# Kernel tuning notes

Measured on AMD Instinct MI355X. Metric: run time of the kernel, lower is better.

Reference implementation:

```python
import jax, jax.numpy as jnp
import numpy as np

D_INPUT, D_MODEL, D_OUTPUT, D_STATE, FACTOR = 100, 256, 100, 64, 2
N2 = D_STATE // 2  # complex conjugate-pair states (S4D)
B_SZ, L_SEQ = 16, 4096


def setup_inputs() -> dict:
    key = jax.random.key(0)
    ks = jax.random.split(key, 12)
    H, N = D_MODEL, N2
    # S4D ('diag-lin', zoh, real_transform='exp') parameters
    log_dt = jax.random.uniform(ks[0], (H,)) * (np.log(0.1) - np.log(0.001)) + np.log(0.001)
    log_A_real = jnp.log(0.5 * jnp.ones((H, N), jnp.float32))
    A_imag = jnp.pi * jnp.broadcast_to(jnp.arange(N, dtype=jnp.float32), (H, N))
    B_re = jnp.ones((H, N), jnp.float32)
    B_im = jnp.zeros((H, N), jnp.float32)
    C_re = jax.random.normal(ks[1], (H, N), jnp.float32)
    C_im = jax.random.normal(ks[2], (H, N), jnp.float32)
    Dskip = jax.random.normal(ks[3], (H,), jnp.float32)
    return {
        'x': jax.random.normal(ks[4], (B_SZ, L_SEQ, D_INPUT), jnp.float32),
        'enc_w': jax.random.normal(ks[5], (D_MODEL, D_INPUT), jnp.float32) / np.sqrt(D_INPUT),
        'enc_b': jnp.zeros((D_MODEL,), jnp.float32),
        'log_dt': log_dt, 'log_A_real': log_A_real, 'A_imag': A_imag,
        'B_re': B_re, 'B_im': B_im, 'C_re': C_re, 'C_im': C_im, 'Dskip': Dskip,
        'ln_g': jnp.ones((D_MODEL,), jnp.float32),
        'ln_b': jnp.zeros((D_MODEL,), jnp.float32),
        'dec1_w': jax.random.normal(ks[6], (D_MODEL * FACTOR, D_MODEL), jnp.float32) / np.sqrt(D_MODEL),
        'dec1_b': jnp.zeros((D_MODEL * FACTOR,), jnp.float32),
        'dec2_w': jax.random.normal(ks[7], (D_OUTPUT, D_MODEL * FACTOR), jnp.float32) / np.sqrt(D_MODEL * FACTOR),
        'dec2_b': jnp.zeros((D_OUTPUT,), jnp.float32),
    }


def s4d_kernel(log_dt, log_A_real, A_imag, B_re, B_im, C_re, C_im, L):
    # diagonal SSM kernel, ZOH discretization: K[h,l] = 2 Re sum_n C'_hn exp(dt_h A_hn)^l
    dt = jnp.exp(log_dt)[:, None]                      # (H,1)
    A = -jnp.exp(log_A_real) + 1j * A_imag             # (H,N)
    C = (B_re + 1j * B_im) * (C_re + 1j * C_im)        # (H,N), B folded into C
    dtA = dt * A                                       # (H,N)
    C = C * (jnp.exp(dtA) - 1.0) / A                   # ZOH correction
    V = jnp.exp(dtA[:, :, None] * jnp.arange(L))       # (H,N,L) Vandermonde
    return 2.0 * jnp.einsum('hn,hnl->hl', C, V).real   # (H,L)


def reference(x, enc_w, enc_b, log_dt, log_A_real, A_imag, B_re, B_im, C_re, C_im,
              Dskip, ln_g, ln_b, dec1_w, dec1_b, dec2_w, dec2_b):
    B, L, _ = x.shape
    u = (x @ enc_w.T + enc_b).transpose(0, 2, 1)       # (B,H,L)
    # FFTConv (single layer), dropout = identity (eval)
    k = s4d_kernel(log_dt, log_A_real, A_imag, B_re, B_im, C_re, C_im, L)
    n = 2 * L
    y = jnp.fft.irfft(jnp.fft.rfft(u, n=n) * jnp.fft.rfft(k, n=n)[None], n=n)[..., :L]
    y = y + u * Dskip[None, :, None]
    y = jax.nn.gelu(y, approximate=False)
    h = y + u                                          # residual
    # LayerNorm over channel dim
    t = h.transpose(0, 2, 1)                           # (B,L,H)
    mu = t.mean(-1, keepdims=True)
    var = jnp.mean((t - mu) ** 2, axis=-1, keepdims=True)
    t = (t - mu) / jnp.sqrt(var + 1e-5) * ln_g + ln_b
    # decoder MLP
    out = jax.nn.gelu(t @ dec1_w.T + dec1_b, approximate=False) @ dec2_w.T + dec2_b
    return out
```

## Files before the change

kernel.cpp:

```cpp
#include <hip/hip_runtime.h>
#include <hip/hip_bf16.h>

#define BB    16
#define LL    4096
#define DIN   100
#define HD    256
#define NN    32
#define DHID  512
#define DOUT  100
#define MROWS (BB*LL)
#define CH    64
#define CC    64
#define NCH   (BB*CC)

#define OFF_WRE    0
#define OFF_WIM    8192
#define OFF_KRE    16384
#define OFF_KIM    24576
#define OFF_WCHR   32768
#define OFF_WCHI   40960
#define OFF_ENCB   49152
#define OFF_DSK    49408
#define OFF_LNG    49664
#define OFF_LNB    49920
#define OFF_B1     50176
#define OFF_B2     50688
#define OFF_WENCB  50816
#define OFF_W1B    67200
#define OFF_W2B    132736
#define OFF_WFL    165504
#define OFF_BY     1230464
#define OFF_VST    2279040
#define OFF_UH     2803328
#define OFF_S      11191936
#define OFF_YH     19580544
#define OFF_TB     OFF_S
#define OFF_G0     OFF_UH
#define OFF_G1     OFF_YH
#define OFF_XB     OFF_YH

typedef __bf16 bf16x8 __attribute__((ext_vector_type(8)));
typedef float  f32x4  __attribute__((ext_vector_type(4)));

static __device__ __forceinline__ int probe_bf16(const void* lng) {
    return ((const unsigned int*)lng)[0] != 0x3f800000u;
}
static __device__ __forceinline__ float ldin(const void* p, long i, int isbf) {
    return isbf ? __bfloat162float(((const __hip_bfloat16*)p)[i]) : ((const float*)p)[i];
}
static __device__ __forceinline__ unsigned short f2bf(float v) {
    union { float f; unsigned u; } c; c.f = v;
    unsigned r = c.u + 0x7fffu + ((c.u >> 16) & 1u);
    return (unsigned short)(r >> 16);
}
static __device__ __forceinline__ float bf2f(unsigned short v) {
    union { unsigned u; float f; } c; c.u = ((unsigned)v) << 16; return c.f;
}
static __device__ __forceinline__ float gelu_f(float x) {
    float z  = fabsf(x) * 0.70710678118654752f;
    float tt = __builtin_amdgcn_rcpf(fmaf(0.3275911f, z, 1.0f));
    float p  = tt * fmaf(tt, fmaf(tt, fmaf(tt, fmaf(tt, 1.061405429f, -1.453152027f),
                          1.421413741f), -0.284496736f), 0.254829592f);
    float er = 1.0f - p * __expf(-z * z);
    return 0.5f * x * (1.0f + copysignf(er, x));
}
static __device__ __forceinline__ void gl2lds16(const unsigned short* g, unsigned short* l) {
    __builtin_amdgcn_global_load_lds(
        (const __attribute__((address_space(1))) unsigned int*)g,
        (__attribute__((address_space(3))) unsigned int*)l, 16, 0, 0);
}

__global__ __launch_bounds__(256) void k_prep(
    const void* encw, const void* encb, const void* logdt, const void* loga,
    const void* aim, const void* bre, const void* bim, const void* cre,
    const void* cim, const void* dsk, const void* lng, const void* lnb,
    const void* w1, const void* b1, const void* w2, const void* b2, float* ws)
{
    const int isbf = probe_bf16(lng);
    unsigned short* WEB = (unsigned short*)(ws + OFF_WENCB);
    unsigned short* W1B = (unsigned short*)(ws + OFF_W1B);
    unsigned short* W2B = (unsigned short*)(ws + OFF_W2B);
    const int total = 8192 + 256*4 + 512 + 128 + 32768 + 131072 + 65536;
    for (int idx = blockIdx.x * blockDim.x + threadIdx.x; idx < total;
         idx += gridDim.x * blockDim.x) {
        int i = idx;
        if (i < 8192) {
            int h = i >> 5;
            float dt  = expf(ldin(logdt, h, isbf));
            float Are = -expf(ldin(loga, i, isbf));
            float Aim = ldin(aim, i, isbf);
            float er  = expf(dt * Are);
            float sv, cv; sincosf(dt * Aim, &sv, &cv);
            float wre = er * cv, wim = er * sv;
            float Bre = ldin(bre, i, isbf), Bim = ldin(bim, i, isbf);
            float Cre = ldin(cre, i, isbf), Cim = ldin(cim, i, isbf);
            float C0re = Bre*Cre - Bim*Cim;
            float C0im = Bre*Cim + Bim*Cre;
            float inv = 1.0f / (Are*Are + Aim*Aim);
            float nre = wre - 1.0f, nim = wim;
            float Zre = (nre*Are + nim*Aim) * inv;
            float Zim = (nim*Are - nre*Aim) * inv;
            float kre = 2.0f * (C0re*Zre - C0im*Zim);
            float kim = -2.0f * (C0re*Zim + C0im*Zre);
            ws[OFF_WRE + i] = wre;  ws[OFF_WIM + i] = wim;
            ws[OFF_KRE + i] = kre;  ws[OFF_KIM + i] = kim;
            float* Wf = ws + OFF_WFL + (long)h * 4160 + 2*(i & 31);
            float pr = 1.0f, pi = 0.0f;
            for (int d = 0; d <= 64; ++d) {
                Wf[d*64]     = pr;
                Wf[d*64 + 1] = pi;
                float tr = pr*wre - pi*wim;
                pi = pr*wim + pi*wre; pr = tr;
            }
            ws[OFF_WCHR + i] = Wf[64*64];
            ws[OFF_WCHI + i] = Wf[64*64 + 1];
        } else if ((i -= 8192) < 256) {
            ws[OFF_ENCB + i] = ldin(encb, i, isbf);
        } else if ((i -= 256) < 256) {
            ws[OFF_DSK + i] = ldin(dsk, i, isbf);
        } else if ((i -= 256) < 256) {
            ws[OFF_LNG + i] = ldin(lng, i, isbf);
        } else if ((i -= 256) < 256) {
            ws[OFF_LNB + i] = ldin(lnb, i, isbf);
        } else if ((i -= 256) < 512) {
            ws[OFF_B1 + i] = ldin(b1, i, isbf);
        } else if ((i -= 512) < 128) {
            ws[OFF_B2 + i] = (i < 100) ? ldin(b2, i, isbf) : 0.0f;
        } else if ((i -= 128) < 32768) {
            int h = i >> 7, k = i & 127;
            WEB[i] = (k < 100) ? f2bf(ldin(encw, (long)h*100 + k, isbf)) : (unsigned short)0;
        } else if ((i -= 32768) < 131072) {
            W1B[i] = f2bf(ldin(w1, i, isbf));
        } else if ((i -= 131072) < 65536) {
            int j = i >> 9, k = i & 511;
            W2B[i] = (j < 100) ? f2bf(ldin(w2, (long)j*512 + k, isbf)) : (unsigned short)0;
        }
    }
}

__global__ __launch_bounds__(256) void k_xcvt(const void* x, const void* lng, float* ws)
{
    const int isbf = probe_bf16(lng);
    unsigned short* Xb = (unsigned short*)(ws + OFF_XB);
    const int total = 65536 * 16;
    for (int s = blockIdx.x * 256 + threadIdx.x; s < total; s += 1024 * 256) {
        int row = s >> 4, slot = s & 15;
        int k0 = slot * 8;
        unsigned short pk[8];
        if (!isbf) {
            const float* xr = (const float*)x + (long)row * 100;
            if (slot < 12) {
                float4 a = *(const float4*)(xr + k0);
                float4 b = *(const float4*)(xr + k0 + 4);
                pk[0]=f2bf(a.x); pk[1]=f2bf(a.y); pk[2]=f2bf(a.z); pk[3]=f2bf(a.w);
                pk[4]=f2bf(b.x); pk[5]=f2bf(b.y); pk[6]=f2bf(b.z); pk[7]=f2bf(b.w);
            } else if (slot == 12) {
                float4 a = *(const float4*)(xr + 96);
                pk[0]=f2bf(a.x); pk[1]=f2bf(a.y); pk[2]=f2bf(a.z); pk[3]=f2bf(a.w);
                pk[4]=0; pk[5]=0; pk[6]=0; pk[7]=0;
            } else {
                #pragma unroll
                for (int j = 0; j < 8; ++j) pk[j] = 0;
            }
        } else {
            const unsigned short* xr = (const unsigned short*)x + (long)row * 100;
            if (slot < 12) {
                *(uint2*)&pk[0] = *(const uint2*)(xr + k0);
                *(uint2*)&pk[4] = *(const uint2*)(xr + k0 + 4);
            } else if (slot == 12) {
                *(uint2*)&pk[0] = *(const uint2*)(xr + 96);
                pk[4]=0; pk[5]=0; pk[6]=0; pk[7]=0;
            } else {
                #pragma unroll
                for (int j = 0; j < 8; ++j) pk[j] = 0;
            }
        }
        *(float4*)&Xb[(long)row * 128 + k0] = *(const float4*)pk;
    }
}

__global__ __launch_bounds__(256) void k_tker(float* ws)
{
    __shared__ float Wp[65*65];
    __shared__ float kr[32], ki[32], Ks[64];
    int h = blockIdx.x;
    int t = threadIdx.x;
    for (int idx = t; idx < 4160; idx += 256) {
        int d = idx >> 6, c = idx & 63;
        Wp[d*65 + c] = ws[OFF_WFL + (long)h*4160 + idx];
    }
    if (t < 32) kr[t] = ws[OFF_KRE + h*32 + t];
    else if (t < 64) ki[t-32] = ws[OFF_KIM + h*32 + (t-32)];
    __syncthreads();
    if (t < 64) {
        float s = 0.0f;
        #pragma unroll
        for (int n = 0; n < 32; ++n)
            s += kr[n]*Wp[t*65 + 2*n] + ki[n]*Wp[t*65 + 2*n + 1];
        Ks[t] = s;
    }
    __syncthreads();
    unsigned short* BY = (unsigned short*)(ws + OFF_BY) + (long)h*8192;
    for (int idx = t; idx < 8192; idx += 256) {
        int j = idx >> 7, k = idx & 127;
        float v;
        if (k < 64) {
            v = (k <= j) ? Ks[j - k] : 0.0f;
        } else {
            int c = k - 64, n = c >> 1;
            float pr = Wp[(j+1)*65 + 2*n], pi = Wp[(j+1)*65 + 2*n + 1];
            v = ((c & 1) == 0) ? (kr[n]*pr + ki[n]*pi) : (ki[n]*pr - kr[n]*pi);
        }
        BY[idx] = f2bf(v);
    }
    unsigned short* Vst = (unsigned short*)(ws + OFF_VST) + (long)h*4096;
    for (int idx = t; idx < 4096; idx += 256) {
        int comp = idx >> 6, i = idx & 63;
        Vst[idx] = f2bf(Wp[(63 - i)*65 + comp]);
    }
}

__global__ __launch_bounds__(256) void k_encm(float* ws)
{
    __shared__ unsigned short SM[32768];
    unsigned short* Cs = SM;
    const unsigned short* Xb  = (const unsigned short*)(ws + OFF_XB);
    const unsigned short* WEB = (const unsigned short*)(ws + OFF_WENCB);
    int bid = blockIdx.x;
    int rt = bid >> 1, ct = bid & 1;
    long row0 = (long)rt * 128;
    int c0 = ct * 128;
    int t = threadIdx.x;
    int lane = t & 63, wv = t >> 6;
    int wm = (wv & 1) * 64, wn = (wv >> 1) * 64;
    int quad = lane >> 4, mr = lane & 15;
    int swz = lane & 7;
    int sr = t >> 3, sdst = (t & 7) * 8, ssrc = ((t & 7) ^ (sr & 7)) * 8;
    f32x4 acc[4][4] = {};
    #pragma unroll
    for (int it = 0; it < 4; ++it) {
        int r = sr + it * 32;
        gl2lds16(&Xb[(row0 + r) * 128 + ssrc], &SM[r * 64 + sdst]);
        gl2lds16(&WEB[(long)(c0 + r) * 128 + ssrc], &SM[8192 + r * 64 + sdst]);
    }
    __syncthreads();
    #pragma unroll
    for (int kc = 0; kc < 2; ++kc) {
        const unsigned short* As = &SM[(kc & 1) * 16384];
        const unsigned short* Bs = As + 8192;
        if (kc == 0) {
            #pragma unroll
            for (int it = 0; it < 4; ++it) {
                int r = sr + it * 32;
                gl2lds16(&Xb[(row0 + r) * 128 + 64 + ssrc], &SM[16384 + r * 64 + sdst]);
                gl2lds16(&WEB[(long)(c0 + r) * 128 + 64 + ssrc], &SM[24576 + r * 64 + sdst]);
            }
        }
        #pragma unroll
        for (int ks = 0; ks < 64; ks += 32) {
            int co = (((ks >> 3) | quad) ^ swz) * 8;
            bf16x8 af[4], bfr[4];
            #pragma unroll
            for (int i = 0; i < 4; ++i)
                af[i] = *(const bf16x8*)&As[(wm + i*16 + mr)*64 + co];
            #pragma unroll
            for (int j = 0; j < 4; ++j)
                bfr[j] = *(const bf16x8*)&Bs[(wn + j*16 + mr)*64 + co];
            #pragma unroll
            for (int i = 0; i < 4; ++i)
                #pragma unroll
                for (int j = 0; j < 4; ++j)
                    acc[i][j] = __builtin_amdgcn_mfma_f32_16x16x32_bf16(af[i], bfr[j], acc[i][j], 0, 0, 0);
        }
        __syncthreads();
    }
    const float* eb = ws + OFF_ENCB;
    #pragma unroll
    for (int j = 0; j < 4; ++j) {
        int hloc = wn + j*16 + mr;
        float bb = eb[c0 + hloc];
        #pragma unroll
        for (int i = 0; i < 4; ++i) {
            int l0 = wm + i*16 + quad*4;
            unsigned short pk[4];
            #pragma unroll
            for (int reg = 0; reg < 4; ++reg)
                pk[reg] = f2bf(acc[i][j][reg] + bb);
            *(uint2*)&Cs[hloc*136 + l0] = *(uint2*)pk;
        }
    }
    __syncthreads();
    unsigned short* Uh = (unsigned short*)(ws + OFF_UH);
    #pragma unroll
    for (int it = 0; it < 8; ++it) {
        int idx = t + it*256;
        int hh = idx >> 4, f = idx & 15;
        *(float4*)&Uh[(long)(c0 + hh)*65536 + row0 + f*8] = *(const float4*)&Cs[hh*136 + f*8];
    }
}

__global__ __launch_bounds__(256) void k_state(float* ws)
{
    __shared__ unsigned short As[128][72];
    __shared__ unsigned short Bs[64][72];
    const unsigned short* Uh  = (const unsigned short*)(ws + OFF_UH);
    const unsigned short* Vst = (const unsigned short*)(ws + OFF_VST);
    int bid = blockIdx.x;
    int h = bid >> 3, ct = bid & 7;
    int c0r = ct * 128;
    int t = threadIdx.x;
    int lane = t & 63, wv = t >> 6;
    int wm = (wv & 1) * 64, wn = (wv >> 1) * 32;
    int quad = lane >> 4, mr = lane & 15;
    const unsigned short* Ubase = Uh + (long)h * 65536;
    #pragma unroll
    for (int it = 0; it < 4; ++it) {
        int idx = t + it*256;
        int r = idx >> 3, f = idx & 7;
        *(float4*)&As[r][f*8] = *(const float4*)&Ubase[(long)(c0r + r)*64 + f*8];
    }
    #pragma unroll
    for (int it = 0; it < 2; ++it) {
        int idx = t + it*256;
        int r = idx >> 3, f = idx & 7;
        *(float4*)&Bs[r][f*8] = *(const float4*)&Vst[(long)h*4096 + r*64 + f*8];
    }
    __syncthreads();
    f32x4 acc[4][2] = {};
    #pragma unroll
    for (int ks = 0; ks < 64; ks += 32) {
        bf16x8 af[4], bfr[2];
        #pragma unroll
        for (int i = 0; i < 4; ++i)
            af[i] = *(const bf16x8*)&As[wm + i*16 + mr][ks + quad*8];
        #pragma unroll
        for (int jn = 0; jn < 2; ++jn)
            bfr[jn] = *(const bf16x8*)&Bs[wn + jn*16 + mr][ks + quad*8];
        #pragma unroll
        for (int i = 0; i < 4; ++i)
            #pragma unroll
            for (int jn = 0; jn < 2; ++jn)
                acc[i][jn] = __builtin_amdgcn_mfma_f32_16x16x32_bf16(af[i], bfr[jn], acc[i][jn], 0, 0, 0);
    }
    __syncthreads();
    unsigned short* Cs = &As[0][0];
    #pragma unroll
    for (int jn = 0; jn < 2; ++jn) {
        int c = wn + jn*16 + mr;
        #pragma unroll
        for (int i = 0; i < 4; ++i)
            #pragma unroll
            for (int reg = 0; reg < 4; ++reg)
                Cs[(wm + i*16 + quad*4 + reg)*72 + c] = f2bf(acc[i][jn][reg]);
    }
    __syncthreads();
    unsigned short* S = (unsigned short*)(ws + OFF_S);
    #pragma unroll
    for (int it = 0; it < 4; ++it) {
        int idx = t + it*256;
        int r = idx >> 3, f = idx & 7;
        *(float4*)&S[(long)(c0r + r)*16384 + h*64 + f*8] = *(const float4*)&Cs[r*72 + f*8];
    }
}

__global__ __launch_bounds__(256) void k_chunk(float* ws)
{
    int tid = blockIdx.x * 256 + threadIdx.x;
    int b = tid >> 13;
    int h = (tid >> 5) & 255;
    int n = tid & 31;
    int i = h * NN + n;
    float wr = ws[OFF_WCHR + i], wi = ws[OFF_WCHI + i];
    unsigned int* Su = (unsigned int*)(ws + OFF_S);
    long a0 = (long)(b * CC) * 8192 + h * 32 + n;
    float rr = 0.0f, ri = 0.0f;
    unsigned int vnext = Su[a0];
    for (int c = 0; c < CC; ++c) {
        long a = a0 + (long)c * 8192;
        unsigned int v = vnext;
        if (c + 1 < CC) vnext = Su[a + 8192];
        float Sr = bf2f((unsigned short)(v & 0xFFFFu));
        float Si = bf2f((unsigned short)(v >> 16));
        Su[a] = (unsigned int)f2bf(rr) | ((unsigned int)f2bf(ri) << 16);
        float nr = fmaf(wr, rr, fmaf(-wi, ri, Sr));
        float ni = fmaf(wr, ri, fmaf(wi, rr, Si));
        rr = nr; ri = ni;
    }
}

__global__ __launch_bounds__(256) void k_y(float* ws)
{
    __shared__ unsigned short As[128][136];
    __shared__ unsigned short Bs[64][136];
    const unsigned short* Uh = (const unsigned short*)(ws + OFF_UH);
    const unsigned short* S  = (const unsigned short*)(ws + OFF_S);
    const unsigned short* BY = (const unsigned short*)(ws + OFF_BY);
    int bid = blockIdx.x;
    int h = bid >> 3, ct = bid & 7;
    int c0r = ct * 128;
    int t = threadIdx.x;
    int lane = t & 63, wv = t >> 6;
    int wm = (wv & 1) * 64, wn = (wv >> 1) * 32;
    int quad = lane >> 4, mr = lane & 15;
    #pragma unroll
    for (int it = 0; it < 8; ++it) {
        int idx = t + it*256;
        int r = idx >> 4, f = idx & 15;
        const unsigned short* src = (f < 8)
            ? &Uh[(long)h*65536 + (long)(c0r + r)*64 + f*8]
            : &S[(long)(c0r + r)*16384 + h*64 + (f-8)*8];
        *(float4*)&As[r][f*8] = *(const float4*)src;
    }
    #pragma unroll
    for (int it = 0; it < 4; ++it) {
        int idx = t + it*256;
        int r = idx >> 4, f = idx & 15;
        *(float4*)&Bs[r][f*8] = *(const float4*)&BY[(long)h*8192 + r*128 + f*8];
    }
    __syncthreads();
    f32x4 acc[4][2] = {};
    #pragma unroll
    for (int ks = 0; ks < 128; ks += 32) {
        bf16x8 af[4], bfr[2];
        #pragma unroll
        for (int i = 0; i < 4; ++i)
            af[i] = *(const bf16x8*)&As[wm + i*16 + mr][ks + quad*8];
        #pragma unroll
        for (int jn = 0; jn < 2; ++jn)
            bfr[jn] = *(const bf16x8*)&Bs[wn + jn*16 + mr][ks + quad*8];
        #pragma unroll
        for (int i = 0; i < 4; ++i)
            #pragma unroll
            for (int jn = 0; jn < 2; ++jn)
                acc[i][jn] = __builtin_amdgcn_mfma_f32_16x16x32_bf16(af[i], bfr[jn], acc[i][jn], 0, 0, 0);
    }
    __syncthreads();
    unsigned short* Cs = &As[0][0];
    #pragma unroll
    for (int jn = 0; jn < 2; ++jn) {
        int c = wn + jn*16 + mr;
        #pragma unroll
        for (int i = 0; i < 4; ++i)
            #pragma unroll
            for (int reg = 0; reg < 4; ++reg)
                Cs[(wm + i*16 + quad*4 + reg)*136 + c] = f2bf(acc[i][jn][reg]);
    }
    __syncthreads();
    unsigned short* Yh = (unsigned short*)(ws + OFF_YH);
    #pragma unroll
    for (int it = 0; it < 4; ++it) {
        int idx = t + it*256;
        int r = idx >> 3, f = idx & 7;
        *(float4*)&Yh[(long)h*65536 + (long)(c0r + r)*64 + f*8] = *(const float4*)&Cs[r*136 + f*8];
    }
}

__global__ __launch_bounds__(1024) void k_ln2(float* ws)
{
    __shared__ unsigned short Vs[64][258];
    __shared__ float parts[64][17], partq[64][17];
    __shared__ float Ms[64], Rs[64];
    __shared__ float Dls[256], Gls[256], Bls[256];
    int chunk = blockIdx.x;
    int t = threadIdx.x;
    if (t < 256) { Dls[t] = ws[OFF_DSK + t]; Gls[t] = ws[OFF_LNG + t]; Bls[t] = ws[OFF_LNB + t]; }
    __syncthreads();
    const unsigned short* Uh = (const unsigned short*)(ws + OFF_UH);
    const unsigned short* Yh = (const unsigned short*)(ws + OFF_YH);
    int j = t & 63, hg = t >> 6;
    float ps = 0.0f, pq = 0.0f;
    #pragma unroll 4
    for (int k = 0; k < 16; ++k) {
        int h = hg*16 + k;
        long base = (long)h*65536 + chunk*64;
        float u = bf2f(Uh[base + j]);
        float y = bf2f(Yh[base + j]);
        float v = gelu_f(fmaf(Dls[h], u, y)) + u;
        Vs[j][h] = f2bf(v);
        ps += v; pq += v*v;
    }
    parts[j][hg] = ps; partq[j][hg] = pq;
    __syncthreads();
    if (t < 64) {
        float s = 0.0f, q = 0.0f;
        #pragma unroll
        for (int g = 0; g < 16; ++g) { s += parts[t][g]; q += partq[t][g]; }
        float mean = s * (1.0f/256.0f);
        float var  = q * (1.0f/256.0f) - mean*mean;
        Ms[t] = mean; Rs[t] = rsqrtf(var + 1e-5f);
    }
    __syncthreads();
    unsigned short* Tb = (unsigned short*)(ws + OFF_TB);
    int h2 = t & 255, jg = t >> 8;
    #pragma unroll 4
    for (int jj = 0; jj < 16; ++jj) {
        int j2 = jg*16 + jj;
        float v = bf2f(Vs[j2][h2]);
        Tb[((long)chunk*64 + j2)*256 + h2] = f2bf((v - Ms[j2]) * Rs[j2] * Gls[h2] + Bls[h2]);
    }
}

__global__ __launch_bounds__(256) void k_dec1m(float* ws)
{
    __shared__ unsigned short SM[16384];
    unsigned short* Cs = SM;
    const unsigned short* Tb  = (const unsigned short*)(ws + OFF_TB);
    const unsigned short* W1B = (const unsigned short*)(ws + OFF_W1B);
    int bid = (blockIdx.x & 7) * 256 + (blockIdx.x >> 3);
    int rt = bid >> 2, ct = bid & 3;
    long row0 = (long)rt * 128;
    int c0 = ct * 128;
    int t = threadIdx.x;
    int lane = t & 63, wv = t >> 6;
    int wm = (wv & 1) * 64, wn = (wv >> 1) * 64;
    int quad = lane >> 4, mr = lane & 15;
    int r1 = t >> 2, c1 = t & 3;
    int r2 = r1 + 64;
    int s1 = (c1 ^ ((r1 & 3) ^ ((r1 >> 2) & 3))) * 8;
    int s2 = (c1 ^ ((r2 & 3) ^ ((r2 >> 2) & 3))) * 8;
    int mrow_a[4], mrow_b[4], coff_a[4], coff_b[4];
    #pragma unroll
    for (int i = 0; i < 4; ++i) {
        int ra = wm + i*16 + mr;
        int rb = wn + i*16 + mr;
        mrow_a[i] = ra * 32; coff_a[i] = (quad ^ ((ra & 3) ^ ((ra >> 2) & 3))) * 8;
        mrow_b[i] = rb * 32; coff_b[i] = (quad ^ ((rb & 3) ^ ((rb >> 2) & 3))) * 8;
    }
    f32x4 acc[4][4] = {};
    gl2lds16(&Tb[(row0 + r1) * 256 + s1], &SM[t * 8]);
    gl2lds16(&Tb[(row0 + r2) * 256 + s2], &SM[2048 + t * 8]);
    gl2lds16(&W1B[(long)(c0 + r1) * 256 + s1], &SM[4096 + t * 8]);
    gl2lds16(&W1B[(long)(c0 + r2) * 256 + s2], &SM[6144 + t * 8]);
    __syncthreads();
    #pragma unroll
    for (int kc = 0; kc < 8; ++kc) {
        const unsigned short* As = &SM[(kc & 1) * 8192];
        const unsigned short* Bs = As + 4096;
        if (kc < 7) {
            int k0 = (kc + 1) * 32;
            unsigned short* D = &SM[((kc + 1) & 1) * 8192];
            gl2lds16(&Tb[(row0 + r1) * 256 + k0 + s1], &D[t * 8]);
            gl2lds16(&Tb[(row0 + r2) * 256 + k0 + s2], &D[2048 + t * 8]);
            gl2lds16(&W1B[(long)(c0 + r1) * 256 + k0 + s1], &D[4096 + t * 8]);
            gl2lds16(&W1B[(long)(c0 + r2) * 256 + k0 + s2], &D[6144 + t * 8]);
        }
        bf16x8 af[4], bfr[4];
        #pragma unroll
        for (int i = 0; i < 4; ++i)
            af[i] = *(const bf16x8*)&As[mrow_a[i] + coff_a[i]];
        #pragma unroll
        for (int j = 0; j < 4; ++j)
            bfr[j] = *(const bf16x8*)&Bs[mrow_b[j] + coff_b[j]];
        #pragma unroll
        for (int i = 0; i < 4; ++i)
            #pragma unroll
            for (int j = 0; j < 4; ++j)
                acc[i][j] = __builtin_amdgcn_mfma_f32_16x16x32_bf16(af[i], bfr[j], acc[i][j], 0, 0, 0);
        __syncthreads();
    }
    const float* b1 = ws + OFF_B1;
    int cswz = quad << 4;
    #pragma unroll
    for (int j = 0; j < 4; ++j) {
        int cloc = wn + j*16 + mr;
        float bb = b1[c0 + cloc];
        int cphys = cloc ^ cswz;
        #pragma unroll
        for (int i = 0; i < 4; ++i)
            #pragma unroll
            for (int reg = 0; reg < 4; ++reg)
                Cs[(wm + i*16 + quad*4 + reg)*128 + cphys] = f2bf(gelu_f(acc[i][j][reg] + bb));
    }
    __syncthreads();
    unsigned short* G = (unsigned short*)(ws + ((ct < 2) ? OFF_G0 : OFF_G1));
    int cl0 = (ct < 2) ? c0 : (c0 - 256);
    #pragma unroll
    for (int it = 0; it < 8; ++it) {
        int idx = t + it*256;
        int r = idx >> 4, f = idx & 15;
        int colp = (f*8) ^ (((r >> 2) & 3) << 4);
        *(float4*)&G[(row0 + r)*256 + cl0 + f*8] = *(const float4*)&Cs[r*128 + colp];
    }
}

__global__ __launch_bounds__(256) void k_dec2m(float* ws, void* out, const void* lng)
{
    const int isbf = probe_bf16(lng);
    __shared__ unsigned short SM[32768];
    unsigned short* Cs = SM;
    const unsigned short* G0  = (const unsigned short*)(ws + OFF_G0);
    const unsigned short* G1  = (const unsigned short*)(ws + OFF_G1);
    const unsigned short* W2B = (const unsigned short*)(ws + OFF_W2B);
    long row0 = (long)blockIdx.x * 128;
    int t = threadIdx.x;
    int lane = t & 63, wv = t >> 6;
    int wm = (wv & 1) * 64, wn = (wv >> 1) * 64;
    int quad = lane >> 4, mr = lane & 15;
    int swz = lane & 7;
    int sr = t >> 3, sdst = (t & 7) * 8, ssrc = ((t & 7) ^ (sr & 7)) * 8;
    f32x4 acc[4][4] = {};
    #pragma unroll
    for (int it = 0; it < 4; ++it) {
        int r = sr + it * 32;
        gl2lds16(&G0[(row0 + r) * 256 + ssrc], &SM[r * 64 + sdst]);
        gl2lds16(&W2B[(long)r * 512 + ssrc], &SM[8192 + r * 64 + sdst]);
    }
    __syncthreads();
    #pragma unroll
    for (int kc = 0; kc < 8; ++kc) {
        const unsigned short* As = &SM[(kc & 1) * 16384];
        const unsigned short* Bs = As + 8192;
        if (kc < 7) {
            int s = kc + 1;
            const unsigned short* Gsrc = (s < 4) ? G0 : G1;
            int kl = (s & 3) * 64;
            int k0 = s * 64;
            unsigned short* Dst = &SM[(s & 1) * 16384];
            #pragma unroll
            for (int it = 0; it < 4; ++it) {
                int r = sr + it * 32;
                gl2lds16(&Gsrc[(row0 + r) * 256 + kl + ssrc], &Dst[r * 64 + sdst]);
                gl2lds16(&W2B[(long)r * 512 + k0 + ssrc], &Dst[8192 + r * 64 + sdst]);
            }
        }
        #pragma unroll
        for (int ks = 0; ks < 64; ks += 32) {
            int co = (((ks >> 3) | quad) ^ swz) * 8;
            bf16x8 af[4], bfr[4];
            #pragma unroll
            for (int i = 0; i < 4; ++i)
                af[i] = *(const bf16x8*)&As[(wm + i*16 + mr)*64 + co];
            #pragma unroll
            for (int j = 0; j < 4; ++j)
                bfr[j] = *(const bf16x8*)&Bs[(wn + j*16 + mr)*64 + co];
            #pragma unroll
            for (int i = 0; i < 4; ++i)
                #pragma unroll
                for (int j = 0; j < 4; ++j)
                    acc[i][j] = __builtin_amdgcn_mfma_f32_16x16x32_bf16(af[i], bfr[j], acc[i][j], 0, 0, 0);
        }
        __syncthreads();
    }
    const float* b2 = ws + OFF_B2;
    if (isbf) {
        #pragma unroll
        for (int j = 0; j < 4; ++j) {
            int cloc = wn + j*16 + mr;
            float bb = b2[cloc];
            #pragma unroll
            for (int i = 0; i < 4; ++i)
                #pragma unroll
                for (int reg = 0; reg < 4; ++reg)
                    Cs[(wm + i*16 + quad*4 + reg)*136 + cloc] = f2bf(acc[i][j][reg] + bb);
        }
        __syncthreads();
        for (int idx = t; idx < 128*25; idx += 256) {
            int r = idx / 25, f = idx % 25;
            uint2* dst = (uint2*)((char*)out + (row0 + r)*200);
            dst[f] = *(const uint2*)&Cs[r*136 + f*4];
        }
    } else {
        #pragma unroll
        for (int j = 0; j < 4; ++j) {
            int col = wn + j*16 + mr;
            if (col < 100) {
                float bb = b2[col];
                #pragma unroll
                for (int i = 0; i < 4; ++i)
                    #pragma unroll
                    for (int reg = 0; reg < 4; ++reg) {
                        long row = row0 + wm + i*16 + quad*4 + reg;
                        ((float*)out)[row * 100 + col] = acc[i][j][reg] + bb;
                    }
            }
        }
    }
}

extern "C" void kernel_launch(void* const* d_in, const int* in_sizes, int n_in,
                              void* d_out, int out_size, void* d_ws, size_t ws_size,
                              hipStream_t stream)
{
    float* ws = (float*)d_ws;
    k_prep<<<512, 256, 0, stream>>>(d_in[1], d_in[2], d_in[3], d_in[4], d_in[5],
                                    d_in[6], d_in[7], d_in[8], d_in[9], d_in[10],
                                    d_in[11], d_in[12], d_in[13], d_in[14],
                                    d_in[15], d_in[16], ws);
    k_xcvt<<<1024, 256, 0, stream>>>(d_in[0], d_in[11], ws);
    k_tker<<<256, 256, 0, stream>>>(ws);
    k_encm<<<1024, 256, 0, stream>>>(ws);
    k_state<<<2048, 256, 0, stream>>>(ws);
    k_chunk<<<512, 256, 0, stream>>>(ws);
    k_y<<<2048, 256, 0, stream>>>(ws);
    k_ln2<<<NCH, 1024, 0, stream>>>(ws);
    k_dec1m<<<2048, 256, 0, stream>>>(ws);
    k_dec2m<<<512, 256, 0, stream>>>(ws, d_out, d_in[11]);
}
```

Measured before the change: 278.4 us.

## Fuse GELU and residual into k_y epilogue; prefetch four chunks in scan

The k_y GEMM epilogue now applies the D-skip, GELU and residual add itself, reusing the u tile already held in shared memory. It writes the activated value in place of the raw convolution output, so k_ln2 no longer re-reads the bf16 u tensor or the D-skip parameters. Separately, the serial chunk-state scan in k_chunk is unrolled by four with a four-deep register prefetch, to hide global-load latency in the recurrence. The fusion depends on the As tile holding u at the matching row and column positions when the epilogue reads it.

```diff
diff --git a/kernel.cpp b/kernel.cpp
--- a/kernel.cpp
+++ b/kernel.cpp
@@ -363,6 +363,15 @@
     }
 }
 
+static __device__ __forceinline__ void chunk_step(unsigned int v, unsigned int* Su,
+        long a, float wr, float wi, float& rr, float& ri) {
+    float Sr = bf2f((unsigned short)(v & 0xFFFFu));
+    float Si = bf2f((unsigned short)(v >> 16));
+    Su[a] = (unsigned int)f2bf(rr) | ((unsigned int)f2bf(ri) << 16);
+    float nr = fmaf(wr, rr, fmaf(-wi, ri, Sr));
+    float ni = fmaf(wr, ri, fmaf(wi, rr, Si));
+    rr = nr; ri = ni;
+}
 __global__ __launch_bounds__(256) void k_chunk(float* ws)
 {
     int tid = blockIdx.x * 256 + threadIdx.x;
@@ -374,17 +383,23 @@
     unsigned int* Su = (unsigned int*)(ws + OFF_S);
     long a0 = (long)(b * CC) * 8192 + h * 32 + n;
     float rr = 0.0f, ri = 0.0f;
-    unsigned int vnext = Su[a0];
-    for (int c = 0; c < CC; ++c) {
+    unsigned int v0 = Su[a0];
+    unsigned int v1 = Su[a0 + 8192];
+    unsigned int v2 = Su[a0 + 2L*8192];
+    unsigned int v3 = Su[a0 + 3L*8192];
+    for (int c = 0; c < CC; c += 4) {
         long a = a0 + (long)c * 8192;
-        unsigned int v = vnext;
-        if (c + 1 < CC) vnext = Su[a + 8192];
-        float Sr = bf2f((unsigned short)(v & 0xFFFFu));
-        float Si = bf2f((unsigned short)(v >> 16));
-        Su[a] = (unsigned int)f2bf(rr) | ((unsigned int)f2bf(ri) << 16);
-        float nr = fmaf(wr, rr, fmaf(-wi, ri, Sr));
-        float ni = fmaf(wr, ri, fmaf(wi, rr, Si));
-        rr = nr; ri = ni;
+        unsigned int u0 = v0, u1 = v1, u2 = v2, u3 = v3;
+        if (c + 4 < CC) {
+            v0 = Su[a + 4L*8192];
+            v1 = Su[a + 5L*8192];
+            v2 = Su[a + 6L*8192];
+            v3 = Su[a + 7L*8192];
+        }
+        chunk_step(u0, Su, a,           wr, wi, rr, ri);
+        chunk_step(u1, Su, a + 8192,    wr, wi, rr, ri);
+        chunk_step(u2, Su, a + 2L*8192, wr, wi, rr, ri);
+        chunk_step(u3, Su, a + 3L*8192, wr, wi, rr, ri);
     }
 }
 
@@ -436,22 +451,27 @@
     }
     __syncthreads();
     unsigned short* Cs = &As[0][0];
+    float Dh = ws[OFF_DSK + h];
     #pragma unroll
     for (int jn = 0; jn < 2; ++jn) {
         int c = wn + jn*16 + mr;
         #pragma unroll
         for (int i = 0; i < 4; ++i)
             #pragma unroll
-            for (int reg = 0; reg < 4; ++reg)
-                Cs[(wm + i*16 + quad*4 + reg)*136 + c] = f2bf(acc[i][jn][reg]);
-    }
-    __syncthreads();
-    unsigned short* Yh = (unsigned short*)(ws + OFF_YH);
+            for (int reg = 0; reg < 4; ++reg) {
+                int row = wm + i*16 + quad*4 + reg;
+                float u = bf2f(Cs[row*136 + c]);
+                float v = gelu_f(fmaf(Dh, u, acc[i][jn][reg])) + u;
+                Cs[row*136 + c] = f2bf(v);
+            }
+    }
+    __syncthreads();
+    unsigned short* Vh = (unsigned short*)(ws + OFF_YH);
     #pragma unroll
     for (int it = 0; it < 4; ++it) {
         int idx = t + it*256;
         int r = idx >> 3, f = idx & 7;
-        *(float4*)&Yh[(long)h*65536 + (long)(c0r + r)*64 + f*8] = *(const float4*)&Cs[r*136 + f*8];
+        *(float4*)&Vh[(long)h*65536 + (long)(c0r + r)*64 + f*8] = *(const float4*)&Cs[r*136 + f*8];
     }
 }
 
@@ -460,23 +480,19 @@
     __shared__ unsigned short Vs[64][258];
     __shared__ float parts[64][17], partq[64][17];
     __shared__ float Ms[64], Rs[64];
-    __shared__ float Dls[256], Gls[256], Bls[256];
+    __shared__ float Gls[256], Bls[256];
     int chunk = blockIdx.x;
     int t = threadIdx.x;
-    if (t < 256) { Dls[t] = ws[OFF_DSK + t]; Gls[t] = ws[OFF_LNG + t]; Bls[t] = ws[OFF_LNB + t]; }
-    __syncthreads();
-    const unsigned short* Uh = (const unsigned short*)(ws + OFF_UH);
-    const unsigned short* Yh = (const unsigned short*)(ws + OFF_YH);
+    if (t < 256) { Gls[t] = ws[OFF_LNG + t]; Bls[t] = ws[OFF_LNB + t]; }
+    const unsigned short* Vh = (const unsigned short*)(ws + OFF_YH);
     int j = t & 63, hg = t >> 6;
     float ps = 0.0f, pq = 0.0f;
     #pragma unroll 4
     for (int k = 0; k < 16; ++k) {
         int h = hg*16 + k;
-        long base = (long)h*65536 + chunk*64;
-        float u = bf2f(Uh[base + j]);
-        float y = bf2f(Yh[base + j]);
-        float v = gelu_f(fmaf(Dls[h], u, y)) + u;
-        Vs[j][h] = f2bf(v);
+        unsigned short raw = Vh[(long)h*65536 + chunk*64 + j];
+        float v = bf2f(raw);
+        Vs[j][h] = raw;
         ps += v; pq += v*v;
     }
     parts[j][hg] = ps; partq[j][hg] = pq;
```

Result: faster. 262.5 us (-5.7%).
